# Performance work log

Hardware: AMD Instinct MI355X
Metric: run time of the kernel (lower is better)

## Reference

```python
import jax, jax.numpy as jnp
import numpy as np

B, NTH, NTW, M, DF = 64, 56, 56, 8, 8
FAR = 100.0  # sentinel location for off sources, as in the torch module


def setup_inputs() -> dict:
    key = jax.random.key(0)
    k1, k2, k3, k4, k5 = jax.random.split(key, 5)
    est_locs = jax.random.uniform(k1, (B, NTH, NTW, M, 2), dtype=jnp.float32)
    true_locs = jax.random.uniform(k2, (B, NTH, NTW, M, 2), dtype=jnp.float32)
    true_fluxes = jax.random.normal(k3, (B, NTH, NTW, M, DF), dtype=jnp.float32)
    est_n_sources = jax.random.randint(k4, (B, NTH, NTW), 0, M + 1, dtype=jnp.int32)
    true_n_sources = jax.random.randint(k5, (B, NTH, NTW), 0, M + 1, dtype=jnp.int32)
    return {"est_locs": est_locs, "true_locs": true_locs, "true_fluxes": true_fluxes,
            "est_n_sources": est_n_sources, "true_n_sources": true_n_sources}


def reference(est_locs, true_locs, true_fluxes, est_n_sources, true_n_sources):
    b, nth, ntw, m, _ = est_locs.shape
    T = b * nth * ntw
    slot = jnp.arange(m)
    # is_on_mask per tile: first n_sources slots are on
    est_on = slot[None, :] < est_n_sources.reshape(T, 1)    # [T, m] bool
    true_on = slot[None, :] < true_n_sources.reshape(T, 1)  # [T, m] bool

    # masked locs -> pairwise L2 distances (torch.cdist p=2)
    el = jnp.where(est_on[..., None], est_locs.reshape(T, m, 2), jnp.float32(FAR))
    tl = jnp.where(true_on[..., None], true_locs.reshape(T, m, 2), jnp.float32(FAR))
    diff = el[:, :, None, :] - tl[:, None, :, :]
    dist = jnp.sqrt(jnp.sum(diff * diff, axis=-1))  # [T, m, m]

    # _fast_one_to_one_match
    match1 = jnp.argmin(dist, axis=1)  # best est row per true col  [T, m]
    match2 = jnp.argmin(dist, axis=2)  # best true col per est row  [T, m]
    match1cond2 = jnp.take_along_axis(match1, match2, axis=1)
    one2one = match1cond2 == slot[None, :]
    est_out = match1 > (est_on.sum(-1, keepdims=True) - 1)
    true_out = match2 > (true_on.sum(-1, keepdims=True) - 1)
    one2one = one2one & ~(est_out | true_out)
    # unmatched pairs point to the padded dump slot m (== est_to_true*mask + offset)
    est_idx = jnp.where(one2one, match1, m)
    true_idx = jnp.where(one2one, match2, m)

    # flat indices across (b*nth*ntw) tiles, each of width m+1
    tile_off = (jnp.arange(T) * (m + 1))[:, None]
    flat_est = (est_idx + tile_off).reshape(-1)
    flat_true = (true_idx + tile_off).reshape(-1)

    # padded true catalog: locs(2) | fluxes(DF) | n_sources-indicator(1)
    fields = jnp.concatenate([
        true_locs.reshape(T, m, 2),
        true_fluxes.reshape(T, m, -1),
        true_on[..., None].astype(jnp.float32),
    ], axis=-1)  # [T, m, 2+DF+1]
    d = fields.shape[-1]
    padded = jnp.concatenate([fields, jnp.zeros((T, 1, d), fields.dtype)], axis=1)
    padded = padded.reshape(T * (m + 1), d)

    # gather matched true rows, scatter into est positions (zeros init)
    target = jnp.zeros_like(padded).at[flat_est].set(padded[flat_true])
    target = target.reshape(T, m + 1, d)[:, :m]  # drop dump slot (v[..., :-1, :])
    return target.reshape(b, nth, ntw, m, d)
```

## Files before the change

### kernel.cpp

```cpp
#include <hip/hip_runtime.h>
#include <math.h>

constexpr int TT = 64 * 56 * 56;
__global__ __launch_bounds__(256) void mvd_coop(
    const float2* __restrict__ el2,
    const float2* __restrict__ tl2,
    const float4* __restrict__ tf4,
    const int*    __restrict__ en_,
    const int*    __restrict__ tn_,
    float4*       __restrict__ out4)
{
#pragma clang fp contract(off)
    const int w    = threadIdx.x >> 6;
    const int L    = threadIdx.x & 63;
    const int tloc = L >> 3;
    const int r    = L & 7;
    const int tb   = blockIdx.x * 32 + w * 8;
    const int gt   = tb + tloc;
    const int g    = gt * 8 + r;

    __shared__ float s_buf[4][704];
    float* sw = s_buf[w];

    const int en = en_[gt];
    const int tn = tn_[gt];

    const float2 eL = el2[g];
    const float2 tL = tl2[g];

    const float ex = (r < en) ? eL.x : 100.0f;
    const float ey = (r < en) ? eL.y : 100.0f;
    const float tx = (r < tn) ? tL.x : 100.0f;
    const float ty = (r < tn) ? tL.y : 100.0f;

    float d[8];
#pragma unroll
    for (int j = 0; j < 8; j++) {
        const float txj = __shfl(tx, j, 8);
        const float tyj = __shfl(ty, j, 8);
        const float dx = ex - txj;
        const float dy = ey - tyj;
        const float dx2 = dx * dx;
        const float dy2 = dy * dy;
        d[j] = sqrtf(dx2 + dy2);
    }

    float rmin = 1e30f; int m2o = 0;
#pragma unroll
    for (int j = 0; j < 8; j++)
        if (d[j] < rmin) { rmin = d[j]; m2o = j; }

    const int gbase = L & 56;
    int m1p = 0;
#pragma unroll
    for (int j = 0; j < 8; j++) {
        float dm = d[j];
#pragma unroll
        for (int s = 1; s < 8; s <<= 1) {
            const float o = __shfl_xor(dm, s);
            dm = (o < dm) ? o : dm;
        }
        const unsigned long long bal = __ballot(d[j] == dm);
        const int b = (int)((bal >> gbase) & 0xFFull);
        m1p |= (__ffs(b) - 1) << (3 * j);
    }

    const int m1r = (m1p >> (3 * r)) & 7;
    const int m1j = (m1p >> (3 * m2o)) & 7;
    const bool o2o = (m1j == r) && (m1r < en) && (m2o < tn);

    const int contrib = o2o ? ((8 | m2o) << (4 * m1r)) : 0;
    const int cmask   = o2o ? (0xF      << (4 * m1r)) : 0;
    int wrd = 0;
#pragma unroll
    for (int s = 0; s < 8; s++) {
        const int cw = __shfl(contrib, s, 8);
        const int cm = __shfl(cmask,  s, 8);
        wrd = (wrd & ~cm) | cw;
    }

    const int  v = (wrd >> (4 * r)) & 15;
    const bool matched = (v & 8) != 0;
    const int  j = v & 7;

    float o0=0,o1=0,o2=0,o3=0,o4=0,o5=0,o6=0,o7=0,o8=0,o9=0,o10=0;
    if (matched) {
        const int sr = gt * 8 + j;
        const float2 p  = tl2[sr];
        const float4 f0 = tf4[2 * sr];
        const float4 f1 = tf4[2 * sr + 1];
        o0 = p.x;  o1 = p.y;
        o2 = f0.x; o3 = f0.y; o4 = f0.z; o5 = f0.w;
        o6 = f1.x; o7 = f1.y; o8 = f1.z; o9 = f1.w;
        o10 = 1.0f;
    }
    {
        float* row = sw + tloc * 88 + r * 11;
        row[0]=o0; row[1]=o1; row[2]=o2; row[3]=o3; row[4]=o4; row[5]=o5;
        row[6]=o6; row[7]=o7; row[8]=o8; row[9]=o9; row[10]=o10;
    }
    __syncthreads();

    const float4* sw4 = (const float4*)sw;
    float4* ob = out4 + (size_t)tb * 22;
#pragma unroll
    for (int k = 0; k < 3; k++) {
        const int fidx = L + 64 * k;
        if (fidx < 176) ob[fidx] = sw4[fidx];
    }
}

extern "C" void kernel_launch(void* const* d_in, const int* in_sizes, int n_in,
                              void* d_out, int out_size, void* d_ws, size_t ws_size,
                              hipStream_t stream) {
    const float* est_locs    = (const float*)d_in[0];
    const float* true_locs   = (const float*)d_in[1];
    const float* true_fluxes = (const float*)d_in[2];
    const int*   est_n       = (const int*)d_in[3];
    const int*   true_n      = (const int*)d_in[4];
    float* out = (float*)d_out;

    mvd_coop<<<TT / 32, 256, 0, stream>>>(
        (const float2*)est_locs, (const float2*)true_locs,
        (const float4*)true_fluxes, est_n, true_n, (float4*)out);
}
```

Baseline: 131.4 us.

## Load fluxes coalesced up front, shuffle matched rows, drop block barrier, nontemporal stores

```diff
diff --git a/kernel.cpp b/kernel.cpp
--- a/kernel.cpp
+++ b/kernel.cpp
@@ -2,6 +2,8 @@
 #include <math.h>
 
 constexpr int TT = 64 * 56 * 56;
+typedef float fx4 __attribute__((ext_vector_type(4)));
+
 __global__ __launch_bounds__(256) void mvd_coop(
     const float2* __restrict__ el2,
     const float2* __restrict__ tl2,
@@ -24,9 +26,10 @@
 
     const int en = en_[gt];
     const int tn = tn_[gt];
-
     const float2 eL = el2[g];
     const float2 tL = tl2[g];
+    const float4 f0 = tf4[2 * g];
+    const float4 f1 = tf4[2 * g + 1];
 
     const float ex = (r < en) ? eL.x : 100.0f;
     const float ey = (r < en) ? eL.y : 100.0f;
@@ -83,30 +86,42 @@
     const bool matched = (v & 8) != 0;
     const int  j = v & 7;
 
-    float o0=0,o1=0,o2=0,o3=0,o4=0,o5=0,o6=0,o7=0,o8=0,o9=0,o10=0;
-    if (matched) {
-        const int sr = gt * 8 + j;
-        const float2 p  = tl2[sr];
-        const float4 f0 = tf4[2 * sr];
-        const float4 f1 = tf4[2 * sr + 1];
-        o0 = p.x;  o1 = p.y;
-        o2 = f0.x; o3 = f0.y; o4 = f0.z; o5 = f0.w;
-        o6 = f1.x; o7 = f1.y; o8 = f1.z; o9 = f1.w;
-        o10 = 1.0f;
-    }
+    const float sx = __shfl(tL.x, j, 8);
+    const float sy = __shfl(tL.y, j, 8);
+    const float s2 = __shfl(f0.x, j, 8);
+    const float s3 = __shfl(f0.y, j, 8);
+    const float s4 = __shfl(f0.z, j, 8);
+    const float s5 = __shfl(f0.w, j, 8);
+    const float s6 = __shfl(f1.x, j, 8);
+    const float s7 = __shfl(f1.y, j, 8);
+    const float s8 = __shfl(f1.z, j, 8);
+    const float s9 = __shfl(f1.w, j, 8);
+
+    const float o0  = matched ? sx : 0.0f;
+    const float o1  = matched ? sy : 0.0f;
+    const float o2  = matched ? s2 : 0.0f;
+    const float o3  = matched ? s3 : 0.0f;
+    const float o4  = matched ? s4 : 0.0f;
+    const float o5  = matched ? s5 : 0.0f;
+    const float o6  = matched ? s6 : 0.0f;
+    const float o7  = matched ? s7 : 0.0f;
+    const float o8  = matched ? s8 : 0.0f;
+    const float o9  = matched ? s9 : 0.0f;
+    const float o10 = matched ? 1.0f : 0.0f;
+
     {
         float* row = sw + tloc * 88 + r * 11;
         row[0]=o0; row[1]=o1; row[2]=o2; row[3]=o3; row[4]=o4; row[5]=o5;
         row[6]=o6; row[7]=o7; row[8]=o8; row[9]=o9; row[10]=o10;
     }
-    __syncthreads();
+    asm volatile("s_waitcnt lgkmcnt(0)" ::: "memory");
 
-    const float4* sw4 = (const float4*)sw;
-    float4* ob = out4 + (size_t)tb * 22;
+    const fx4* sw4 = (const fx4*)sw;
+    fx4* ob = (fx4*)(out4 + (size_t)tb * 22);
 #pragma unroll
     for (int k = 0; k < 3; k++) {
         const int fidx = L + 64 * k;
-        if (fidx < 176) ob[fidx] = sw4[fidx];
+        if (fidx < 176) __builtin_nontemporal_store(sw4[fidx], &ob[fidx]);
     }
 }
 
```

Result: no change. 133.9 us (+1.9%).
